# Kernel tuning notes

Hardware: AMD Instinct MI355X
Metric: run time of the kernel (lower is better)

Reference implementation:

```python
import jax, jax.numpy as jnp
import numpy as np

NUM_FREQ = 32
MAX_POS = 10000.0
COORD_DIM = 3
EMB_DIM = COORD_DIM * NUM_FREQ * 2  # 192
KIN = 2 * EMB_DIM                   # 384
C = 32
T = 4
N_Y = 50000
N_X = 32768
K = 8
E = N_X * K
MLP_DIMS = [KIN, 128, 256, 128, C]


def sinusoidal_embed(p):
    # transformer-style sinusoidal embedding: [n, d] -> [n, d*NUM_FREQ*2]
    freqs = (1.0 / MAX_POS) ** (jnp.arange(NUM_FREQ, dtype=p.dtype) / NUM_FREQ)
    ang = p[..., None] * freqs                       # [n, d, nf]
    emb = jnp.stack([jnp.sin(ang), jnp.cos(ang)], axis=-1)  # [n, d, nf, 2]
    return emb.reshape(p.shape[0], -1)


def setup_inputs() -> dict:
    key = jax.random.key(0)
    ks = jax.random.split(key, 16)
    inp = {
        "y": jax.random.uniform(ks[0], (N_Y, COORD_DIM), dtype=jnp.float32),
        "x": jax.random.uniform(ks[1], (N_X, COORD_DIM), dtype=jnp.float32),
        "f_y": jax.random.normal(ks[2], (T, N_Y, C), dtype=jnp.float32),
        "neighbors_index": jax.random.randint(ks[3], (E,), 0, N_Y, dtype=jnp.int64),
    }
    # channel MLP params: 384 -> 128 -> 256 -> 128 -> 32, gelu between layers
    for i in range(4):
        fan_in, fan_out = MLP_DIMS[i], MLP_DIMS[i + 1]
        s = 1.0 / np.sqrt(fan_in)
        inp[f"W{i}"] = jax.random.uniform(ks[4 + 2 * i], (fan_in, fan_out), jnp.float32, -s, s)
        inp[f"b{i}"] = jax.random.uniform(ks[5 + 2 * i], (fan_out,), jnp.float32, -s, s)
    return inp


def reference(y, x, f_y, neighbors_index, W0, b0, W1, b1, W2, b2, W3, b3):
    n_x = x.shape[0]
    k = neighbors_index.shape[0] // n_x
    y_emb = sinusoidal_embed(y)            # [n_y, 192]
    x_emb = sinusoidal_embed(x)            # [n_x, 192]
    rep = y_emb[neighbors_index]           # [E, 192] gather per edge
    slf = jnp.repeat(x_emb, k, axis=0)     # [E, 192] query embedding per edge
    h = jnp.concatenate([rep, slf], axis=-1)  # [E, 384]
    h = jax.nn.gelu(h @ W0 + b0)
    h = jax.nn.gelu(h @ W1 + b1)
    h = jax.nn.gelu(h @ W2 + b2)
    kern = h @ W3 + b3                     # [E, C] kernel values
    in_feat = f_y[:, neighbors_index, :]   # [T, E, C] gathered source features
    prod = kern[None, :, :] * in_feat      # linear transform: k(x,y) * f(y)
    # reduction='sum' over each query's neighborhood (uniform K segments)
    out = prod.reshape(f_y.shape[0], n_x, k, -1).sum(axis=2)  # [T, n_x, C]
    return out
```

## Files before the change

### kernel.cpp

```cpp
#include <hip/hip_runtime.h>
#include <stdint.h>

#define EMB_DIM 192
#define CDIM 32
#define TDIM 4
#define N_Y 50000
#define N_X 32768
#define KNBR 8
#define ECNT (N_X*KNBR)

#define H1S 134
#define H2S 262
#define KS  33
#define ES  200

#define PREP_CY 782
#define PREP_CX 512
#define PREP_CNB (PREP_CY + PREP_CX)

#define PREP_WNB 464

typedef __attribute__((ext_vector_type(8))) short bf16x8;
typedef __attribute__((ext_vector_type(4))) float f32x4;

static __device__ __forceinline__ short f2bf(float f){
  unsigned u = __float_as_uint(f);
  return (short)((u + 0x7FFFu) >> 16);
}
static __device__ __forceinline__ unsigned pk_bf16(float lo, float hi){
  return ((__float_as_uint(lo) + 0x7FFFu) >> 16) |
         ((((__float_as_uint(hi) + 0x7FFFu) >> 16)) << 16);
}
static __device__ __forceinline__ float geluf(float x){
  float x2 = x * x;
  float u  = __builtin_fmaf(0.044715f, x2, 1.0f);
  float p  = x * -1.5957691216057308f;
  float e  = __expf(p * u);
  return x * __builtin_amdgcn_rcpf(1.0f + e);
}

__global__ __launch_bounds__(256) void prep_w(
    const float* __restrict__ W0, const float* __restrict__ W1,
    const float* __restrict__ W2, const float* __restrict__ W3,
    short* __restrict__ w0t, short* __restrict__ w1t,
    short* __restrict__ w2t, short* __restrict__ w3t)
{
  int id = blockIdx.x * 256 + threadIdx.x;
  if (id < 49152) {
    int k = id >> 7, n = id & 127;
    w0t[n * 384 + k] = f2bf(W0[(size_t)k * 128 + n]);
  } else if (id < 81920) {
    int loc = id - 49152; int n = loc >> 7, k = loc & 127;
    w1t[loc] = f2bf(W1[k * 256 + n]);
  } else if (id < 114688) {
    int loc = id - 81920; int n = loc >> 8, k = loc & 255;
    w2t[loc] = f2bf(W2[k * 128 + n]);
  } else if (id < 118784) {
    int loc = id - 114688; int n = loc >> 7, k = loc & 127;
    w3t[loc] = f2bf(W3[k * 32 + n]);
  }
}

__global__ __launch_bounds__(256, 2) void prep_c(
    const float* __restrict__ ypts, const float* __restrict__ xpts,
    const short* __restrict__ w0t, const float* __restrict__ b0,
    short* __restrict__ c_y, float* __restrict__ c_x)
{
  __shared__ __attribute__((aligned(16))) short s_e[64 * ES];
  const int tid = threadIdx.x;
  const bool isY = blockIdx.x < PREP_CY;
  const int row0 = isY ? blockIdx.x * 64 : (blockIdx.x - PREP_CY) * 64;
  const int wave = tid >> 6, lane = tid & 63;
  const int quad = lane >> 4, l15 = lane & 15;
  const short* w0h = w0t + (isY ? 0 : 192);

  bf16x8 bv[2][6];
  #pragma unroll
  for (int nt = 0; nt < 2; ++nt) {
    int n = wave * 32 + nt * 16 + l15;
    #pragma unroll
    for (int ch = 0; ch < 6; ++ch)
      bv[nt][ch] = *(const bf16x8*)&w0h[(size_t)n * 384 + ch * 32 + quad * 8];
  }

  {
    const int r = tid >> 2, q = tid & 3;
    const int grow = row0 + r;
    const bool valid = isY ? (grow < N_Y) : true;
    const float* src = isY ? (ypts + (size_t)grow * 3) : (xpts + (size_t)grow * 3);
    float c[3] = {0.f, 0.f, 0.f};
    if (valid) { c[0] = src[0]; c[1] = src[1]; c[2] = src[2]; }
    #pragma unroll
    for (int j = 0; j < 24; ++j) {
      int p = q * 24 + j;
      int d = p >> 5, i = p & 31;
      float f = __expf(-0.28782313662425575f * (float)i);
      float rev = c[d] * f * 0.15915494309189535f;
      float s  = __builtin_amdgcn_sinf(rev);
      float co = __builtin_amdgcn_cosf(rev);
      *(unsigned*)&s_e[r * ES + d * 64 + 2 * i] = pk_bf16(s, co);
    }
  }
  __syncthreads();

  f32x4 acc[4][2];
  #pragma unroll
  for (int mt = 0; mt < 4; ++mt)
    #pragma unroll
    for (int nt = 0; nt < 2; ++nt) acc[mt][nt] = (f32x4){0.f, 0.f, 0.f, 0.f};
  #pragma unroll
  for (int ch = 0; ch < 6; ++ch) {
    bf16x8 a[4];
    #pragma unroll
    for (int mt = 0; mt < 4; ++mt)
      a[mt] = *(const bf16x8*)&s_e[(mt * 16 + l15) * ES + ch * 32 + quad * 8];
    #pragma unroll
    for (int mt = 0; mt < 4; ++mt)
      #pragma unroll
      for (int nt = 0; nt < 2; ++nt)
        acc[mt][nt] = __builtin_amdgcn_mfma_f32_16x16x32_bf16(
            a[mt], bv[nt][ch], acc[mt][nt], 0, 0, 0);
  }
  #pragma unroll
  for (int nt = 0; nt < 2; ++nt) {
    int col = wave * 32 + nt * 16 + l15;
    float bias = isY ? 0.f : b0[col];
    #pragma unroll
    for (int mt = 0; mt < 4; ++mt)
      #pragma unroll
      for (int rg = 0; rg < 4; ++rg) {
        int grow = row0 + mt * 16 + quad * 4 + rg;
        if (isY) { if (grow < N_Y) c_y[(size_t)grow * 128 + col] = f2bf(acc[mt][nt][rg]); }
        else     { c_x[(size_t)grow * 128 + col] = acc[mt][nt][rg] + bias; }
      }
  }
}

__global__ __launch_bounds__(256, 3) void fused_edge(
    const short* __restrict__ c_y, const float* __restrict__ c_x,
    const int* __restrict__ nidx, const float* __restrict__ f_y,
    const short* __restrict__ w1t, const float* __restrict__ b1,
    const short* __restrict__ w2t, const float* __restrict__ b2,
    const short* __restrict__ w3t, const float* __restrict__ b3,
    float* __restrict__ out)
{
  __shared__ __attribute__((aligned(16))) char smem[50688];
  short* s_h2   = (short*)smem;
  float* s_kern = (float*)smem;
  short* s_h1   = (short*)(smem + 33536);

  const int tid  = threadIdx.x;
  const int e0   = blockIdx.x * 64;
  const int wave = tid >> 6, lane = tid & 63;
  const int quad = lane >> 4, l15 = lane & 15;

  {
    const int r = tid >> 2, q = tid & 3;
    const int idx = nidx[e0 + r];
    const uint4*  cyp = (const uint4*)(c_y + (size_t)idx * 128 + q * 32);
    const float4* cxp = (const float4*)(c_x + (size_t)((e0 + r) >> 3) * 128 + q * 32);
    uint4  cyv[4];
    float4 cxv[8];
    #pragma unroll
    for (int i = 0; i < 4; ++i) cyv[i] = cyp[i];
    #pragma unroll
    for (int i = 0; i < 8; ++i) cxv[i] = cxp[i];
    const float* cxa = (const float*)cxv;
    const unsigned* cya = (const unsigned*)cyv;
    unsigned pk[16];
    #pragma unroll
    for (int jj = 0; jj < 16; ++jj) {
      unsigned u = cya[jj];
      float lo = __uint_as_float(u << 16)         + cxa[2 * jj];
      float hi = __uint_as_float(u & 0xffff0000u) + cxa[2 * jj + 1];
      pk[jj] = pk_bf16(geluf(lo), geluf(hi));
    }
    uint4* dst = (uint4*)&s_h1[r * H1S + q * 32];
    #pragma unroll
    for (int jj = 0; jj < 4; ++jj)
      dst[jj] = *(uint4*)&pk[jj * 4];
  }
  __syncthreads();

  {
    f32x4 acc1[4][4];
    #pragma unroll
    for (int mt = 0; mt < 4; ++mt)
      #pragma unroll
      for (int nt = 0; nt < 4; ++nt) acc1[mt][nt] = (f32x4){0.f, 0.f, 0.f, 0.f};
    #pragma unroll
    for (int ch = 0; ch < 4; ++ch) {
      bf16x8 a[4], b[4];
      #pragma unroll
      for (int mt = 0; mt < 4; ++mt)
        a[mt] = *(const bf16x8*)&s_h1[(mt * 16 + l15) * H1S + ch * 32 + quad * 8];
      #pragma unroll
      for (int nt = 0; nt < 4; ++nt)
        b[nt] = *(const bf16x8*)&w1t[(size_t)(wave * 64 + nt * 16 + l15) * 128 + ch * 32 + quad * 8];
      #pragma unroll
      for (int mt = 0; mt < 4; ++mt)
        #pragma unroll
        for (int nt = 0; nt < 4; ++nt)
          acc1[mt][nt] = __builtin_amdgcn_mfma_f32_16x16x32_bf16(a[mt], b[nt], acc1[mt][nt], 0, 0, 0);
    }
    #pragma unroll
    for (int nt = 0; nt < 4; ++nt) {
      int col = wave * 64 + nt * 16 + l15;
      float bias = b1[col];
      #pragma unroll
      for (int mt = 0; mt < 4; ++mt)
        #pragma unroll
        for (int rg = 0; rg < 4; ++rg) {
          int row = mt * 16 + quad * 4 + rg;
          s_h2[row * H2S + col] = f2bf(geluf(acc1[mt][nt][rg] + bias));
        }
    }
  }
  __syncthreads();

  {
    f32x4 acc2[4][2];
    #pragma unroll
    for (int mt = 0; mt < 4; ++mt)
      #pragma unroll
      for (int nt = 0; nt < 2; ++nt) acc2[mt][nt] = (f32x4){0.f, 0.f, 0.f, 0.f};
    #pragma unroll
    for (int ch = 0; ch < 8; ++ch) {
      bf16x8 a[4], b[2];
      #pragma unroll
      for (int mt = 0; mt < 4; ++mt)
        a[mt] = *(const bf16x8*)&s_h2[(mt * 16 + l15) * H2S + ch * 32 + quad * 8];
      #pragma unroll
      for (int nt = 0; nt < 2; ++nt)
        b[nt] = *(const bf16x8*)&w2t[(size_t)(wave * 32 + nt * 16 + l15) * 256 + ch * 32 + quad * 8];
      #pragma unroll
      for (int mt = 0; mt < 4; ++mt)
        #pragma unroll
        for (int nt = 0; nt < 2; ++nt)
          acc2[mt][nt] = __builtin_amdgcn_mfma_f32_16x16x32_bf16(a[mt], b[nt], acc2[mt][nt], 0, 0, 0);
    }
    #pragma unroll
    for (int nt = 0; nt < 2; ++nt) {
      int col = wave * 32 + nt * 16 + l15;
      float bias = b2[col];
      #pragma unroll
      for (int mt = 0; mt < 4; ++mt)
        #pragma unroll
        for (int rg = 0; rg < 4; ++rg) {
          int row = mt * 16 + quad * 4 + rg;
          s_h1[row * H1S + col] = f2bf(geluf(acc2[mt][nt][rg] + bias));
        }
    }
  }
  __syncthreads();

  {
    f32x4 acc3[2];
    acc3[0] = (f32x4){0.f, 0.f, 0.f, 0.f};
    acc3[1] = (f32x4){0.f, 0.f, 0.f, 0.f};
    #pragma unroll
    for (int ch = 0; ch < 4; ++ch) {
      bf16x8 a3 = *(const bf16x8*)&s_h1[(wave * 16 + l15) * H1S + ch * 32 + quad * 8];
      #pragma unroll
      for (int nt = 0; nt < 2; ++nt) {
        bf16x8 b3f = *(const bf16x8*)&w3t[(size_t)(nt * 16 + l15) * 128 + ch * 32 + quad * 8];
        acc3[nt] = __builtin_amdgcn_mfma_f32_16x16x32_bf16(a3, b3f, acc3[nt], 0, 0, 0);
      }
    }
    #pragma unroll
    for (int nt = 0; nt < 2; ++nt) {
      int col = nt * 16 + l15;
      float bias = b3[col];
      #pragma unroll
      for (int rg = 0; rg < 4; ++rg) {
        int row = wave * 16 + quad * 4 + rg;
        s_kern[row * KS + col] = acc3[nt][rg] + bias;
      }
    }
  }
  __syncthreads();

  {
    const int xloc = tid >> 5;
    const int c    = tid & 31;
    float acc[TDIM] = {0.f, 0.f, 0.f, 0.f};
    const int ebase = xloc * 8;
    #pragma unroll
    for (int j = 0; j < KNBR; ++j) {
      float kv = s_kern[(ebase + j) * KS + c];
      int idx = nidx[e0 + ebase + j];
      const float* fp = f_y + (size_t)idx * CDIM + c;
      #pragma unroll
      for (int t = 0; t < TDIM; ++t)
        acc[t] += kv * fp[(size_t)t * N_Y * CDIM];
    }
    const int xg = blockIdx.x * 8 + xloc;
    #pragma unroll
    for (int t = 0; t < TDIM; ++t)
      out[((size_t)t * N_X + xg) * CDIM + c] = acc[t];
  }
}

extern "C" void kernel_launch(void* const* d_in, const int* in_sizes, int n_in,
                              void* d_out, int out_size, void* d_ws, size_t ws_size,
                              hipStream_t stream)
{
  const float* y   = (const float*)d_in[0];
  const float* x   = (const float*)d_in[1];
  const float* f_y = (const float*)d_in[2];
  const int*  nidx = (const int*)d_in[3];
  const float* W0 = (const float*)d_in[4];  const float* b0 = (const float*)d_in[5];
  const float* W1 = (const float*)d_in[6];  const float* b1 = (const float*)d_in[7];
  const float* W2 = (const float*)d_in[8];  const float* b2 = (const float*)d_in[9];
  const float* W3 = (const float*)d_in[10]; const float* b3 = (const float*)d_in[11];

  char* ws = (char*)d_ws;
  short* c_y  = (short*)(ws + 0);
  float* c_x  = (float*)(ws + 12800000);
  short* w1t  = (short*)(ws + 29577216);
  short* w2t  = (short*)(ws + 29642752);
  short* w3t  = (short*)(ws + 29708288);
  short* w0t  = (short*)(ws + 29716480);

  hipLaunchKernelGGL(prep_w, dim3(PREP_WNB), dim3(256), 0, stream,
                     W0, W1, W2, W3, w0t, w1t, w2t, w3t);
  hipLaunchKernelGGL(prep_c, dim3(PREP_CNB), dim3(256), 0, stream,
                     y, x, w0t, b0, c_y, c_x);
  hipLaunchKernelGGL(fused_edge, dim3(ECNT / 64), dim3(256), 0, stream,
                     c_y, c_x, nidx, f_y, w1t, b1, w2t, b2, w3t, b3, (float*)d_out);
}
```

Before: 241.7 us.

## Prefetch f_y gathers before MLP layers and fold GELU constants into exp2

```diff
diff --git a/kernel.cpp b/kernel.cpp
--- a/kernel.cpp
+++ b/kernel.cpp
@@ -33,9 +33,8 @@
 }
 static __device__ __forceinline__ float geluf(float x){
   float x2 = x * x;
-  float u  = __builtin_fmaf(0.044715f, x2, 1.0f);
-  float p  = x * -1.5957691216057308f;
-  float e  = __expf(p * u);
+  float w  = __builtin_fmaf(x2, -0.10294324f, -2.3022082f);
+  float e  = __builtin_amdgcn_exp2f(x * w);
   return x * __builtin_amdgcn_rcpf(1.0f + e);
 }
 
@@ -145,6 +144,7 @@
     float* __restrict__ out)
 {
   __shared__ __attribute__((aligned(16))) char smem[50688];
+  __shared__ int s_nidx[64];
   short* s_h2   = (short*)smem;
   float* s_kern = (float*)smem;
   short* s_h1   = (short*)(smem + 33536);
@@ -153,10 +153,12 @@
   const int e0   = blockIdx.x * 64;
   const int wave = tid >> 6, lane = tid & 63;
   const int quad = lane >> 4, l15 = lane & 15;
+  const int xloc = tid >> 5, cc = tid & 31;
 
   {
     const int r = tid >> 2, q = tid & 3;
     const int idx = nidx[e0 + r];
+    if (q == 0) s_nidx[r] = idx;
     const uint4*  cyp = (const uint4*)(c_y + (size_t)idx * 128 + q * 32);
     const float4* cxp = (const float4*)(c_x + (size_t)((e0 + r) >> 3) * 128 + q * 32);
     uint4  cyv[4];
@@ -182,6 +184,16 @@
   }
   __syncthreads();
 
+  float fv[KNBR][TDIM];
+  #pragma unroll
+  for (int j = 0; j < KNBR; ++j) {
+    int idxj = s_nidx[xloc * 8 + j];
+    const float* fp = f_y + (size_t)idxj * CDIM + cc;
+    #pragma unroll
+    for (int t = 0; t < TDIM; ++t)
+      fv[j][t] = fp[(size_t)t * (N_Y * CDIM)];
+  }
+
   {
     f32x4 acc1[4][4];
     #pragma unroll
@@ -216,6 +228,11 @@
         }
     }
   }
+  #pragma unroll
+  for (int j = 0; j < KNBR; ++j)
+    #pragma unroll
+    for (int t = 0; t < TDIM; ++t)
+      asm volatile("" :: "v"(fv[j][t]));
   __syncthreads();
 
   {
@@ -281,23 +298,19 @@
   __syncthreads();
 
   {
-    const int xloc = tid >> 5;
-    const int c    = tid & 31;
     float acc[TDIM] = {0.f, 0.f, 0.f, 0.f};
     const int ebase = xloc * 8;
     #pragma unroll
     for (int j = 0; j < KNBR; ++j) {
-      float kv = s_kern[(ebase + j) * KS + c];
-      int idx = nidx[e0 + ebase + j];
-      const float* fp = f_y + (size_t)idx * CDIM + c;
+      float kv = s_kern[(ebase + j) * KS + cc];
       #pragma unroll
       for (int t = 0; t < TDIM; ++t)
-        acc[t] += kv * fp[(size_t)t * N_Y * CDIM];
+        acc[t] += kv * fv[j][t];
     }
     const int xg = blockIdx.x * 8 + xloc;
     #pragma unroll
     for (int t = 0; t < TDIM; ++t)
-      out[((size_t)t * N_X + xg) * CDIM + c] = acc[t];
+      out[((size_t)t * N_X + xg) * CDIM + cc] = acc[t];
   }
 }
 
```

After: 237.5 us (median of 3 runs). About the same (-1.7%).

## Restructure edge MLP to per-wave independent tiles without block barriers

Applied to the files above, without the earlier changes.

```diff
diff --git a/kernel.cpp b/kernel.cpp
--- a/kernel.cpp
+++ b/kernel.cpp
@@ -9,9 +9,6 @@
 #define KNBR 8
 #define ECNT (N_X*KNBR)
 
-#define H1S 134
-#define H2S 262
-#define KS  33
 #define ES  200
 
 #define PREP_CY 782
@@ -23,6 +20,8 @@
 typedef __attribute__((ext_vector_type(8))) short bf16x8;
 typedef __attribute__((ext_vector_type(4))) float f32x4;
 
+#define MEMFENCE() asm volatile("" ::: "memory")
+
 static __device__ __forceinline__ short f2bf(float f){
   unsigned u = __float_as_uint(f);
   return (short)((u + 0x7FFFu) >> 16);
@@ -33,10 +32,15 @@
 }
 static __device__ __forceinline__ float geluf(float x){
   float x2 = x * x;
-  float u  = __builtin_fmaf(0.044715f, x2, 1.0f);
-  float p  = x * -1.5957691216057308f;
-  float e  = __expf(p * u);
+  float w  = __builtin_fmaf(x2, -0.10294324f, -2.3022082f);
+  float e  = __builtin_amdgcn_exp2f(x * w);
   return x * __builtin_amdgcn_rcpf(1.0f + e);
+}
+static __device__ __forceinline__ bf16x8 mk8(unsigned a, unsigned b,
+                                             unsigned c, unsigned d){
+  union { unsigned u[4]; bf16x8 v; } t;
+  t.u[0] = a; t.u[1] = b; t.u[2] = c; t.u[3] = d;
+  return t.v;
 }
 
 __global__ __launch_bounds__(256) void prep_w(
@@ -144,160 +148,157 @@
     const short* __restrict__ w3t, const float* __restrict__ b3,
     float* __restrict__ out)
 {
-  __shared__ __attribute__((aligned(16))) char smem[50688];
-  short* s_h2   = (short*)smem;
-  float* s_kern = (float*)smem;
-  short* s_h1   = (short*)(smem + 33536);
+  __shared__ __attribute__((aligned(16))) char smem[4 * 8192 + 4 * 64];
 
   const int tid  = threadIdx.x;
-  const int e0   = blockIdx.x * 64;
   const int wave = tid >> 6, lane = tid & 63;
-  const int quad = lane >> 4, l15 = lane & 15;
-
+  const int g = lane >> 4, j = lane & 15;
+  const int swz = (j & 7) << 4;
+  const int ew0 = blockIdx.x * 64 + wave * 16;
+  char* buf   = smem + wave * 8192;
+  int* s_idxw = (int*)(smem + 4 * 8192) + wave * 16;
+
+  const int idxj = nidx[ew0 + j];
+  if (g == 0) s_idxw[j] = idxj;
+  const int xj = (ew0 + j) >> 3;
+
+  bf16x8 b1f[4];
   {
-    const int r = tid >> 2, q = tid & 3;
-    const int idx = nidx[e0 + r];
-    const uint4*  cyp = (const uint4*)(c_y + (size_t)idx * 128 + q * 32);
-    const float4* cxp = (const float4*)(c_x + (size_t)((e0 + r) >> 3) * 128 + q * 32);
-    uint4  cyv[4];
-    float4 cxv[8];
-    #pragma unroll
-    for (int i = 0; i < 4; ++i) cyv[i] = cyp[i];
-    #pragma unroll
-    for (int i = 0; i < 8; ++i) cxv[i] = cxp[i];
-    const float* cxa = (const float*)cxv;
-    const unsigned* cya = (const unsigned*)cyv;
-    unsigned pk[16];
-    #pragma unroll
-    for (int jj = 0; jj < 16; ++jj) {
-      unsigned u = cya[jj];
-      float lo = __uint_as_float(u << 16)         + cxa[2 * jj];
-      float hi = __uint_as_float(u & 0xffff0000u) + cxa[2 * jj + 1];
-      pk[jj] = pk_bf16(geluf(lo), geluf(hi));
-    }
-    uint4* dst = (uint4*)&s_h1[r * H1S + q * 32];
-    #pragma unroll
-    for (int jj = 0; jj < 4; ++jj)
-      dst[jj] = *(uint4*)&pk[jj * 4];
-  }
-  __syncthreads();
+    const short* cyr = c_y + (size_t)idxj * 128;
+    const float* cxr = c_x + (size_t)xj * 128;
+    #pragma unroll
+    for (int ch = 0; ch < 4; ++ch) {
+      int k0 = ch * 32 + g * 8;
+      uint4  cy  = *(const uint4*)&cyr[k0];
+      float4 cx0 = *(const float4*)&cxr[k0];
+      float4 cx1 = *(const float4*)&cxr[k0 + 4];
+      float cxs[8] = {cx0.x, cx0.y, cx0.z, cx0.w, cx1.x, cx1.y, cx1.z, cx1.w};
+      const unsigned* cya = (const unsigned*)&cy;
+      unsigned pk[4];
+      #pragma unroll
+      for (int s2 = 0; s2 < 4; ++s2) {
+        unsigned u = cya[s2];
+        float lo = __uint_as_float(u << 16)         + cxs[2 * s2];
+        float hi = __uint_as_float(u & 0xffff0000u) + cxs[2 * s2 + 1];
+        pk[s2] = pk_bf16(geluf(lo), geluf(hi));
+      }
+      b1f[ch] = mk8(pk[0], pk[1], pk[2], pk[3]);
+    }
+  }
+
+  f32x4 acc1[16];
+  #pragma unroll
+  for (int nt = 0; nt < 16; ++nt) acc1[nt] = (f32x4){0.f, 0.f, 0.f, 0.f};
+  #pragma unroll
+  for (int nt = 0; nt < 16; ++nt)
+    #pragma unroll
+    for (int ch = 0; ch < 4; ++ch) {
+      bf16x8 a = *(const bf16x8*)&w1t[(size_t)(nt * 16 + j) * 128 + ch * 32 + g * 8];
+      acc1[nt] = __builtin_amdgcn_mfma_f32_16x16x32_bf16(a, b1f[ch], acc1[nt], 0, 0, 0);
+    }
+
+  const int xloc = lane >> 5, cc = lane & 31;
+  int eidx[8];
+  #pragma unroll
+  for (int jj = 0; jj < 8; ++jj) eidx[jj] = s_idxw[xloc * 8 + jj];
+  float fv[8][TDIM];
+  #pragma unroll
+  for (int jj = 0; jj < 8; ++jj) {
+    const float* fp = f_y + (size_t)eidx[jj] * CDIM + cc;
+    #pragma unroll
+    for (int t = 0; t < TDIM; ++t)
+      fv[jj][t] = fp[(size_t)t * (N_Y * CDIM)];
+  }
+
+  #pragma unroll
+  for (int nt = 0; nt < 16; ++nt) {
+    const float4 bb = *(const float4*)&b1[nt * 16 + 4 * g];
+    float v0 = geluf(acc1[nt][0] + bb.x);
+    float v1 = geluf(acc1[nt][1] + bb.y);
+    float v2 = geluf(acc1[nt][2] + bb.z);
+    float v3 = geluf(acc1[nt][3] + bb.w);
+    uint2 w; w.x = pk_bf16(v0, v1); w.y = pk_bf16(v2, v3);
+    *(uint2*)(buf + j * 512 + ((nt * 32 + 8 * g) ^ swz)) = w;
+  }
+  MEMFENCE();
+
+  bf16x8 b2f[8];
+  #pragma unroll
+  for (int ch2 = 0; ch2 < 8; ++ch2)
+    b2f[ch2] = *(const bf16x8*)(buf + j * 512 + ((ch2 * 64 + g * 16) ^ swz));
+  MEMFENCE();
+
+  f32x4 acc2[8];
+  #pragma unroll
+  for (int nt = 0; nt < 8; ++nt) acc2[nt] = (f32x4){0.f, 0.f, 0.f, 0.f};
+  #pragma unroll
+  for (int nt = 0; nt < 8; ++nt)
+    #pragma unroll
+    for (int ch2 = 0; ch2 < 8; ++ch2) {
+      bf16x8 a = *(const bf16x8*)&w2t[(size_t)(nt * 16 + j) * 256 + ch2 * 32 + g * 8];
+      acc2[nt] = __builtin_amdgcn_mfma_f32_16x16x32_bf16(a, b2f[ch2], acc2[nt], 0, 0, 0);
+    }
+
+  #pragma unroll
+  for (int jj = 0; jj < 8; ++jj)
+    #pragma unroll
+    for (int t = 0; t < TDIM; ++t)
+      asm volatile("" :: "v"(fv[jj][t]));
+
+  #pragma unroll
+  for (int nt = 0; nt < 8; ++nt) {
+    const float4 bb = *(const float4*)&b2[nt * 16 + 4 * g];
+    float v0 = geluf(acc2[nt][0] + bb.x);
+    float v1 = geluf(acc2[nt][1] + bb.y);
+    float v2 = geluf(acc2[nt][2] + bb.z);
+    float v3 = geluf(acc2[nt][3] + bb.w);
+    uint2 w; w.x = pk_bf16(v0, v1); w.y = pk_bf16(v2, v3);
+    *(uint2*)(buf + j * 512 + ((nt * 32 + 8 * g) ^ swz)) = w;
+  }
+  MEMFENCE();
+
+  bf16x8 b3f[4];
+  #pragma unroll
+  for (int ch3 = 0; ch3 < 4; ++ch3)
+    b3f[ch3] = *(const bf16x8*)(buf + j * 512 + ((ch3 * 64 + g * 16) ^ swz));
+  MEMFENCE();
+
+  f32x4 acc3[2];
+  acc3[0] = (f32x4){0.f, 0.f, 0.f, 0.f};
+  acc3[1] = (f32x4){0.f, 0.f, 0.f, 0.f};
+  #pragma unroll
+  for (int nt = 0; nt < 2; ++nt)
+    #pragma unroll
+    for (int ch3 = 0; ch3 < 4; ++ch3) {
+      bf16x8 a = *(const bf16x8*)&w3t[(size_t)(nt * 16 + j) * 128 + ch3 * 32 + g * 8];
+      acc3[nt] = __builtin_amdgcn_mfma_f32_16x16x32_bf16(a, b3f[ch3], acc3[nt], 0, 0, 0);
+    }
+
+  #pragma unroll
+  for (int nt = 0; nt < 2; ++nt) {
+    const float4 bb = *(const float4*)&b3[nt * 16 + 4 * g];
+    float4 w;
+    w.x = acc3[nt][0] + bb.x;
+    w.y = acc3[nt][1] + bb.y;
+    w.z = acc3[nt][2] + bb.z;
+    w.w = acc3[nt][3] + bb.w;
+    *(float4*)(buf + (j * 36 + nt * 16 + 4 * g) * 4) = w;
+  }
+  MEMFENCE();
 
   {
-    f32x4 acc1[4][4];
-    #pragma unroll
-    for (int mt = 0; mt < 4; ++mt)
-      #pragma unroll
-      for (int nt = 0; nt < 4; ++nt) acc1[mt][nt] = (f32x4){0.f, 0.f, 0.f, 0.f};
-    #pragma unroll
-    for (int ch = 0; ch < 4; ++ch) {
-      bf16x8 a[4], b[4];
-      #pragma unroll
-      for (int mt = 0; mt < 4; ++mt)
-        a[mt] = *(const bf16x8*)&s_h1[(mt * 16 + l15) * H1S + ch * 32 + quad * 8];
-      #pragma unroll
-      for (int nt = 0; nt < 4; ++nt)
-        b[nt] = *(const bf16x8*)&w1t[(size_t)(wave * 64 + nt * 16 + l15) * 128 + ch * 32 + quad * 8];
-      #pragma unroll
-      for (int mt = 0; mt < 4; ++mt)
-        #pragma unroll
-        for (int nt = 0; nt < 4; ++nt)
-          acc1[mt][nt] = __builtin_amdgcn_mfma_f32_16x16x32_bf16(a[mt], b[nt], acc1[mt][nt], 0, 0, 0);
-    }
-    #pragma unroll
-    for (int nt = 0; nt < 4; ++nt) {
-      int col = wave * 64 + nt * 16 + l15;
-      float bias = b1[col];
-      #pragma unroll
-      for (int mt = 0; mt < 4; ++mt)
-        #pragma unroll
-        for (int rg = 0; rg < 4; ++rg) {
-          int row = mt * 16 + quad * 4 + rg;
-          s_h2[row * H2S + col] = f2bf(geluf(acc1[mt][nt][rg] + bias));
-        }
-    }
-  }
-  __syncthreads();
-
-  {
-    f32x4 acc2[4][2];
-    #pragma unroll
-    for (int mt = 0; mt < 4; ++mt)
-      #pragma unroll
-      for (int nt = 0; nt < 2; ++nt) acc2[mt][nt] = (f32x4){0.f, 0.f, 0.f, 0.f};
-    #pragma unroll
-    for (int ch = 0; ch < 8; ++ch) {
-      bf16x8 a[4], b[2];
-      #pragma unroll
-      for (int mt = 0; mt < 4; ++mt)
-        a[mt] = *(const bf16x8*)&s_h2[(mt * 16 + l15) * H2S + ch * 32 + quad * 8];
-      #pragma unroll
-      for (int nt = 0; nt < 2; ++nt)
-        b[nt] = *(const bf16x8*)&w2t[(size_t)(wave * 32 + nt * 16 + l15) * 256 + ch * 32 + quad * 8];
-      #pragma unroll
-      for (int mt = 0; mt < 4; ++mt)
-        #pragma unroll
-        for (int nt = 0; nt < 2; ++nt)
-          acc2[mt][nt] = __builtin_amdgcn_mfma_f32_16x16x32_bf16(a[mt], b[nt], acc2[mt][nt], 0, 0, 0);
-    }
-    #pragma unroll
-    for (int nt = 0; nt < 2; ++nt) {
-      int col = wave * 32 + nt * 16 + l15;
-      float bias = b2[col];
-      #pragma unroll
-      for (int mt = 0; mt < 4; ++mt)
-        #pragma unroll
-        for (int rg = 0; rg < 4; ++rg) {
-          int row = mt * 16 + quad * 4 + rg;
-          s_h1[row * H1S + col] = f2bf(geluf(acc2[mt][nt][rg] + bias));
-        }
-    }
-  }
-  __syncthreads();
-
-  {
-    f32x4 acc3[2];
-    acc3[0] = (f32x4){0.f, 0.f, 0.f, 0.f};
-    acc3[1] = (f32x4){0.f, 0.f, 0.f, 0.f};
-    #pragma unroll
-    for (int ch = 0; ch < 4; ++ch) {
-      bf16x8 a3 = *(const bf16x8*)&s_h1[(wave * 16 + l15) * H1S + ch * 32 + quad * 8];
-      #pragma unroll
-      for (int nt = 0; nt < 2; ++nt) {
-        bf16x8 b3f = *(const bf16x8*)&w3t[(size_t)(nt * 16 + l15) * 128 + ch * 32 + quad * 8];
-        acc3[nt] = __builtin_amdgcn_mfma_f32_16x16x32_bf16(a3, b3f, acc3[nt], 0, 0, 0);
-      }
-    }
-    #pragma unroll
-    for (int nt = 0; nt < 2; ++nt) {
-      int col = nt * 16 + l15;
-      float bias = b3[col];
-      #pragma unroll
-      for (int rg = 0; rg < 4; ++rg) {
-        int row = wave * 16 + quad * 4 + rg;
-        s_kern[row * KS + col] = acc3[nt][rg] + bias;
-      }
-    }
-  }
-  __syncthreads();
-
-  {
-    const int xloc = tid >> 5;
-    const int c    = tid & 31;
     float acc[TDIM] = {0.f, 0.f, 0.f, 0.f};
-    const int ebase = xloc * 8;
-    #pragma unroll
-    for (int j = 0; j < KNBR; ++j) {
-      float kv = s_kern[(ebase + j) * KS + c];
-      int idx = nidx[e0 + ebase + j];
-      const float* fp = f_y + (size_t)idx * CDIM + c;
+    #pragma unroll
+    for (int jj = 0; jj < 8; ++jj) {
+      float kv = *(const float*)(buf + ((xloc * 8 + jj) * 36 + cc) * 4);
       #pragma unroll
       for (int t = 0; t < TDIM; ++t)
-        acc[t] += kv * fp[(size_t)t * N_Y * CDIM];
-    }
-    const int xg = blockIdx.x * 8 + xloc;
+        acc[t] += kv * fv[jj][t];
+    }
+    const int xg = (ew0 >> 3) + xloc;
     #pragma unroll
     for (int t = 0; t < TDIM; ++t)
-      out[((size_t)t * N_X + xg) * CDIM + c] = acc[t];
+      out[((size_t)t * N_X + xg) * CDIM + cc] = acc[t];
   }
 }
 
```

Result: slower. 379.8 us (+57.2%).
